# Kernel optimization log

Hardware: AMD Instinct MI355X
Metric: run time of the kernel (lower is better)

## Reference

```python
import jax, jax.numpy as jnp
import numpy as np

N_NODES = 50000
N_EDGES = 800000


def setup_inputs() -> dict:
    key = jax.random.key(0)
    ks = jax.random.split(key, 8)
    x = jax.random.normal(ks[0], (N_NODES, 256), dtype=jnp.float32)
    edge_index = jax.random.randint(ks[1], (2, N_EDGES), 0, N_NODES, dtype=jnp.int64)
    edge_weight = jax.random.uniform(ks[2], (N_EDGES,), dtype=jnp.float32)
    # Glorot-style weights for the 3 GCNConv layers: 256->128->64->32
    def glorot(k, fan_in, fan_out):
        s = jnp.sqrt(6.0 / (fan_in + fan_out))
        return jax.random.uniform(k, (fan_in, fan_out), dtype=jnp.float32, minval=-s, maxval=s)
    return {
        "x": x,
        "edge_index": edge_index,
        "edge_weight": edge_weight,
        "W1": glorot(ks[3], 256, 128), "b1": jnp.zeros((128,), jnp.float32),
        "W2": glorot(ks[4], 128, 64),  "b2": jnp.zeros((64,), jnp.float32),
        "W3": glorot(ks[5], 64, 32),   "b3": jnp.zeros((32,), jnp.float32),
    }


def _gcn_forward(x, row, col, ew, params):
    """Stacked GCNConv+ReLU (PyG semantics: add self loops, symmetric norm)."""
    n = x.shape[0]
    loop = jnp.arange(n, dtype=row.dtype)
    row_f = jnp.concatenate([row, loop])            # [E+N] sources
    col_f = jnp.concatenate([col, loop])            # [E+N] targets
    ew_f = jnp.concatenate([ew, jnp.ones((n,), ew.dtype)])
    deg = jax.ops.segment_sum(ew_f, col_f, num_segments=n)
    dinv = jnp.where(deg > 0, jax.lax.rsqrt(deg), 0.0)
    norm = dinv[row_f] * ew_f * dinv[col_f]         # [E+N]
    for W, b in params:
        h = x @ W                                   # [N, d_out] linear first (PyG order)
        msg = h[row_f] * norm[:, None]              # [E+N, d_out] gather + scale
        agg = jax.ops.segment_sum(msg, col_f, num_segments=n)  # scatter-add
        x = jax.nn.relu(agg + b)                    # fused bias + ReLU
    return x


def reference(x, edge_index, edge_weight, W1, b1, W2, b2, W3, b3):
    row, col = edge_index[0], edge_index[1]
    params = [(W1, b1), (W2, b2), (W3, b3)]
    return _gcn_forward(x, row, col, edge_weight, params)
```

## Files before the change

kernel.cpp:

```cpp
#include <hip/hip_runtime.h>
#include <hip/hip_fp16.h>


#define D0 256
#define D1 128
#define D2 64
#define D3 32

#define FIX_SCALE 16777216.0f
#define FIX_INV   (1.0f / 16777216.0f)

typedef _Float16 half8 __attribute__((ext_vector_type(8)));
typedef float floatx4 __attribute__((ext_vector_type(4)));

__global__ __launch_bounds__(256) void hist_kernel(
        const int* __restrict__ ei, const float* __restrict__ ew,
        unsigned long long* __restrict__ pk, int* __restrict__ rank, int E) {
    int e = blockIdx.x * 256 + threadIdx.x;
    if (e < E) {
        int c = ei[E + e];
        unsigned int wfix = (unsigned int)(ew[e] * FIX_SCALE + 0.5f);
        unsigned long long old =
            atomicAdd(&pk[c], (1ULL << 32) | (unsigned long long)wfix);
        rank[e] = (int)(old >> 32);
    }
}

__global__ __launch_bounds__(256) void scan_reduce(const unsigned long long* __restrict__ pk,
                                                   float* __restrict__ dinv,
                                                   int* __restrict__ cnt,
                                                   int* __restrict__ blockSum, int N) {
    __shared__ int s[256];
    const int t = threadIdx.x;
    const int i = blockIdx.x * 256 + t;
    int v = 0;
    if (i < N) {
        unsigned long long p = pk[i];
        float d = (float)(unsigned int)(p & 0xffffffffULL) * FIX_INV + 1.0f;
        dinv[i] = rsqrtf(d);
        v = (int)(p >> 32);
        cnt[i] = v;
    }
    s[t] = v;
    __syncthreads();
#pragma unroll
    for (int off = 128; off > 0; off >>= 1) {
        if (t < off) s[t] += s[t + off];
        __syncthreads();
    }
    if (t == 0) blockSum[blockIdx.x] = s[0];
}

__global__ __launch_bounds__(256) void scan_apply(const int* __restrict__ cnt,
                                                  const int* __restrict__ blockSum,
                                                  int* __restrict__ row_ptr, int N, int B) {
    __shared__ int bs[256];
    __shared__ int s[256];
    const int t = threadIdx.x;
    bs[t] = (t < B) ? blockSum[t] : 0;
    __syncthreads();
#pragma unroll
    for (int off = 1; off < 256; off <<= 1) {
        int u = (t >= off) ? bs[t - off] : 0;
        __syncthreads();
        bs[t] += u;
        __syncthreads();
    }
    const int myOff = (blockIdx.x > 0) ? bs[blockIdx.x - 1] : 0;
    const int i = blockIdx.x * 256 + t;
    const int v = (i < N) ? cnt[i] : 0;
    s[t] = v;
    __syncthreads();
#pragma unroll
    for (int off = 1; off < 256; off <<= 1) {
        int u = (t >= off) ? s[t - off] : 0;
        __syncthreads();
        s[t] += u;
        __syncthreads();
    }
    if (i < N) row_ptr[i] = s[t] - v + myOff;
    if (blockIdx.x == 0 && t == 0) row_ptr[N] = bs[B - 1];
}

__device__ __forceinline__ void stage_slab(const float* __restrict__ X, int slab,
                                           _Float16 (*__restrict__ sA)[D0 + 8], int t) {
    const int row = t >> 4;
    const int c0 = (t & 15) * 16;
    const float* src = X + (size_t)(slab * 16 + row) * D0 + c0;
    float4 f0 = *(const float4*)(src + 0);
    float4 f1 = *(const float4*)(src + 4);
    float4 f2 = *(const float4*)(src + 8);
    float4 f3 = *(const float4*)(src + 12);
    half8 h0, h1;
    h0[0] = (_Float16)f0.x; h0[1] = (_Float16)f0.y;
    h0[2] = (_Float16)f0.z; h0[3] = (_Float16)f0.w;
    h0[4] = (_Float16)f1.x; h0[5] = (_Float16)f1.y;
    h0[6] = (_Float16)f1.z; h0[7] = (_Float16)f1.w;
    h1[0] = (_Float16)f2.x; h1[1] = (_Float16)f2.y;
    h1[2] = (_Float16)f2.z; h1[3] = (_Float16)f2.w;
    h1[4] = (_Float16)f3.x; h1[5] = (_Float16)f3.y;
    h1[6] = (_Float16)f3.z; h1[7] = (_Float16)f3.w;
    *(half8*)&sA[row][c0]     = h0;
    *(half8*)&sA[row][c0 + 8] = h1;
}

__global__ __launch_bounds__(256) void fillgemm_kernel(
        const float* __restrict__ x, const float* __restrict__ W1,
        _Float16* __restrict__ h1, int N,
        const int* __restrict__ ei, const float* __restrict__ ew,
        const float* __restrict__ dinv, const int* __restrict__ row_ptr,
        const int* __restrict__ rank, int2* __restrict__ pairs, int E, int gB) {
    __shared__ _Float16 sA[2][16][D0 + 8];
    const int b = blockIdx.x;
    if (b >= gB) {
        int e = (b - gB) * 256 + threadIdx.x;
        if (e < E) {
            int r = ei[e];
            int c = ei[E + e];
            float w = dinv[r] * ew[e] * dinv[c];
            pairs[row_ptr[c] + rank[e]] = make_int2(r, __float_as_int(w));
        }
        return;
    }
    constexpr int NC = D0 / 32;
    const int tid = threadIdx.x;
    const int w = tid >> 6;
    const int lane = tid & 63;
    const int quad = lane >> 4;
    const int m = lane & 15;
    const int n0 = w * 32;

    half8 b0[NC], b1[NC];
#pragma unroll
    for (int c = 0; c < NC; ++c) {
#pragma unroll
        for (int j = 0; j < 8; ++j) {
            int k = c * 32 + quad * 8 + j;
            b0[c][j] = (_Float16)W1[(size_t)k * D1 + n0 + m];
            b1[c][j] = (_Float16)W1[(size_t)k * D1 + n0 + 16 + m];
        }
    }

    const int nslab = N >> 4;
    int slab = b;
    if (slab >= nslab) return;
    stage_slab(x, slab, sA[0], tid);
    __syncthreads();
    int buf = 0;
    while (true) {
        const int next = slab + gB;
        if (next < nslab) stage_slab(x, next, sA[buf ^ 1], tid);

        half8 a[NC];
#pragma unroll
        for (int c = 0; c < NC; ++c)
            a[c] = *(const half8*)&sA[buf][m][c * 32 + quad * 8];
        floatx4 acc0 = (floatx4){0.f, 0.f, 0.f, 0.f};
        floatx4 acc1 = (floatx4){0.f, 0.f, 0.f, 0.f};
#pragma unroll
        for (int c = 0; c < NC; ++c) {
            acc0 = __builtin_amdgcn_mfma_f32_16x16x32_f16(a[c], b0[c], acc0, 0, 0, 0);
            acc1 = __builtin_amdgcn_mfma_f32_16x16x32_f16(a[c], b1[c], acc1, 0, 0, 0);
        }

        const int r0 = slab * 16 + quad * 4;
#pragma unroll
        for (int r = 0; r < 4; ++r) {
            h1[(size_t)(r0 + r) * D1 + n0 + m]      = (_Float16)acc0[r];
            h1[(size_t)(r0 + r) * D1 + n0 + 16 + m] = (_Float16)acc1[r];
        }
        __syncthreads();
        if (next >= nslab) break;
        slab = next;
        buf ^= 1;
    }
}

template <int DIN, int DOUT>
__global__ __launch_bounds__(256) void agg_gemm_kernel(
        const _Float16* __restrict__ H, const int* __restrict__ row_ptr,
        const int2* __restrict__ pairs, const float* __restrict__ dinv,
        const float* __restrict__ bias, const float* __restrict__ W,
        _Float16* __restrict__ Hout, int N) {
    constexpr int TPN = DIN / 8;
    constexpr int NPB = 256 / TPN;
    constexpr int NC  = DIN / 32;
    constexpr int S   = NPB / 16;
    constexpr int T   = DOUT / 16;
    static_assert(S * T == 4, "one tile per wave");
    __shared__ _Float16 sA[NPB][DIN + 8];

    const int tid = threadIdx.x;
    const int g = tid / TPN;
    const int sl = tid % TPN;
    const int node0 = blockIdx.x * NPB;
    const int node = node0 + g;
    const bool valid = node < N;

    const int w = tid >> 6;
    const int lane = tid & 63;
    const int q = lane >> 4;
    const int m = lane & 15;
    const int s = w & (S - 1);
    const int t = w / S;
    half8 bf[NC];
#pragma unroll
    for (int c = 0; c < NC; ++c) {
#pragma unroll
        for (int j = 0; j < 8; ++j)
            bf[c][j] = (_Float16)W[(size_t)(c * 32 + q * 8 + j) * DOUT + t * 16 + m];
    }

    float acc[8];
#pragma unroll
    for (int j = 0; j < 8; ++j) acc[j] = 0.0f;

    int beg = 0, end = 0;
    float di = 0.f;
    half8 uself = (half8){0,0,0,0,0,0,0,0};
    float bb[8];
    if (valid) {
        beg = row_ptr[node];
        end = row_ptr[node + 1];
        di = dinv[node];
        uself = *(const half8*)&H[(size_t)node * DIN + sl * 8];
        *(float4*)&bb[0] = *(const float4*)&bias[sl * 8];
        *(float4*)&bb[4] = *(const float4*)&bias[sl * 8 + 4];
    }

    if (end > beg) {
        const int last = end - 1;
        int2 p0 = pairs[beg];
        int2 p1 = pairs[min(beg + 1, last)];
        int2 p2 = pairs[min(beg + 2, last)];
        int2 p3 = pairs[min(beg + 3, last)];
        int2 p4 = pairs[min(beg + 4, last)];
        half8 u0 = *(const half8*)&H[(size_t)p0.x * DIN + sl * 8];
        half8 u1 = *(const half8*)&H[(size_t)p1.x * DIN + sl * 8];
        half8 u2 = *(const half8*)&H[(size_t)p2.x * DIN + sl * 8];
        half8 u3 = *(const half8*)&H[(size_t)p3.x * DIN + sl * 8];
        for (int k = beg; k < end; ++k) {
            int2 p5 = pairs[min(k + 5, last)];
            half8 u4 = *(const half8*)&H[(size_t)p4.x * DIN + sl * 8];
            float wv = __int_as_float(p0.y);
#pragma unroll
            for (int j = 0; j < 8; ++j) acc[j] = fmaf(wv, (float)u0[j], acc[j]);
            p0 = p1; p1 = p2; p2 = p3; p3 = p4; p4 = p5;
            u0 = u1; u1 = u2; u2 = u3; u3 = u4;
        }
    }

    if (valid) {
        float d2 = di * di;
#pragma unroll
        for (int j = 0; j < 8; ++j) acc[j] = fmaf(d2, (float)uself[j], acc[j]);
        half8 o;
#pragma unroll
        for (int j = 0; j < 8; ++j) o[j] = (_Float16)fmaxf(acc[j] + bb[j], 0.f);
        *(half8*)&sA[g][sl * 8] = o;
    }
    __syncthreads();

    half8 a[NC];
#pragma unroll
    for (int c = 0; c < NC; ++c)
        a[c] = *(const half8*)&sA[s * 16 + m][c * 32 + q * 8];
    floatx4 o4 = (floatx4){0.f, 0.f, 0.f, 0.f};
#pragma unroll
    for (int c = 0; c < NC; ++c)
        o4 = __builtin_amdgcn_mfma_f32_16x16x32_f16(a[c], bf[c], o4, 0, 0, 0);
#pragma unroll
    for (int r = 0; r < 4; ++r) {
        const int nr = node0 + s * 16 + q * 4 + r;
        if (nr < N) Hout[(size_t)nr * DOUT + t * 16 + m] = (_Float16)o4[r];
    }
}

template <int D, typename OUT>
__global__ __launch_bounds__(256) void agg_kernel(const _Float16* __restrict__ H,
                                                  const int* __restrict__ row_ptr,
                                                  const int2* __restrict__ pairs,
                                                  const float* __restrict__ dinv,
                                                  const float* __restrict__ bias,
                                                  OUT* __restrict__ out, int N) {
    constexpr int TPN = D / 8;
    constexpr int NPB = 256 / TPN;
    const int tid = threadIdx.x;
    const int g = tid / TPN;
    const int lane = tid % TPN;
    const int node = blockIdx.x * NPB + g;
    if (node >= N) return;

    const int beg = row_ptr[node];
    const int end = row_ptr[node + 1];
    const float di = dinv[node];
    const half8 uself = *(const half8*)&H[(size_t)node * D + lane * 8];
    float b[8];
    *(float4*)&b[0] = *(const float4*)&bias[lane * 8];
    *(float4*)&b[4] = *(const float4*)&bias[lane * 8 + 4];

    float acc[8];
#pragma unroll
    for (int j = 0; j < 8; ++j) acc[j] = 0.0f;

    if (end > beg) {
        const int last = end - 1;
        int2 p0 = pairs[beg];
        int2 p1 = pairs[min(beg + 1, last)];
        int2 p2 = pairs[min(beg + 2, last)];
        int2 p3 = pairs[min(beg + 3, last)];
        int2 p4 = pairs[min(beg + 4, last)];
        half8 u0 = *(const half8*)&H[(size_t)p0.x * D + lane * 8];
        half8 u1 = *(const half8*)&H[(size_t)p1.x * D + lane * 8];
        half8 u2 = *(const half8*)&H[(size_t)p2.x * D + lane * 8];
        half8 u3 = *(const half8*)&H[(size_t)p3.x * D + lane * 8];
        for (int k = beg; k < end; ++k) {
            int2 p5 = pairs[min(k + 5, last)];
            half8 u4 = *(const half8*)&H[(size_t)p4.x * D + lane * 8];
            float w = __int_as_float(p0.y);
#pragma unroll
            for (int j = 0; j < 8; ++j) acc[j] = fmaf(w, (float)u0[j], acc[j]);
            p0 = p1; p1 = p2; p2 = p3; p3 = p4; p4 = p5;
            u0 = u1; u1 = u2; u2 = u3; u3 = u4;
        }
    }
    const float d2 = di * di;
#pragma unroll
    for (int j = 0; j < 8; ++j) acc[j] = fmaf(d2, (float)uself[j], acc[j]);
#pragma unroll
    for (int j = 0; j < 8; ++j) acc[j] = fmaxf(acc[j] + b[j], 0.f);

    if constexpr (sizeof(OUT) == 2) {
        half8 o;
#pragma unroll
        for (int j = 0; j < 8; ++j) o[j] = (_Float16)acc[j];
        *(half8*)&out[(size_t)node * D + lane * 8] = o;
    } else {
        float* dst = (float*)&out[(size_t)node * D + lane * 8];
        *(float4*)&dst[0] = make_float4(acc[0], acc[1], acc[2], acc[3]);
        *(float4*)&dst[4] = make_float4(acc[4], acc[5], acc[6], acc[7]);
    }
}

extern "C" void kernel_launch(void* const* d_in, const int* in_sizes, int n_in,
                              void* d_out, int out_size, void* d_ws, size_t ws_size,
                              hipStream_t stream) {
    const float* x   = (const float*)d_in[0];
    const int* ei    = (const int*)d_in[1];
    const float* ew  = (const float*)d_in[2];
    const float* W1  = (const float*)d_in[3];
    const float* b1  = (const float*)d_in[4];
    const float* W2  = (const float*)d_in[5];
    const float* b2  = (const float*)d_in[6];
    const float* W3  = (const float*)d_in[7];
    const float* b3  = (const float*)d_in[8];
    float* out = (float*)d_out;

    const int N = in_sizes[0] / D0;
    const int E = in_sizes[2];
    (void)n_in; (void)out_size; (void)ws_size;

    char* ws = (char*)d_ws;
    size_t off = 0;
    auto carve = [&](size_t bytes) -> void* {
        void* p = (void*)(ws + off);
        off += (bytes + 255) & ~(size_t)255;
        return p;
    };
    unsigned long long* pk = (unsigned long long*)carve((size_t)N * 8);
    float* dinv    = (float*)carve((size_t)N * 4);
    int*   cnt     = (int*)carve((size_t)N * 4);
    int*   row_ptr = (int*)carve((size_t)(N + 1) * 4);
    int*   rank    = (int*)carve((size_t)E * 4);
    int*   bsum    = (int*)carve(256 * 4);
    int2*  pairs   = (int2*)carve((size_t)E * 8);
    _Float16* bufH = (_Float16*)carve((size_t)N * D1 * 2);
    _Float16* bufO = (_Float16*)carve((size_t)N * D1 * 2);

    _Float16* h1 = bufH;
    _Float16* h2 = bufO;
    _Float16* h3 = bufH;

    const int eb = (E + 255) / 256;
    const int scanB = (N + 255) / 256;
    const int gB = 768;

    hipMemsetAsync(pk, 0, (size_t)N * 8, stream);
    hist_kernel<<<eb, 256, 0, stream>>>(ei, ew, pk, rank, E);

    scan_reduce<<<scanB, 256, 0, stream>>>(pk, dinv, cnt, bsum, N);
    scan_apply<<<scanB, 256, 0, stream>>>(cnt, bsum, row_ptr, N, scanB);

    fillgemm_kernel<<<gB + eb, 256, 0, stream>>>(
        x, W1, h1, N, ei, ew, dinv, row_ptr, rank, pairs, E, gB);

    agg_gemm_kernel<D1, D2><<<(N + 15) / 16, 256, 0, stream>>>(
        h1, row_ptr, pairs, dinv, b1, W2, h2, N);

    agg_gemm_kernel<D2, D3><<<(N + 31) / 32, 256, 0, stream>>>(
        h2, row_ptr, pairs, dinv, b2, W3, h3, N);

    agg_kernel<D3, float><<<(N + 63) / 64, 256, 0, stream>>>(
        h3, row_ptr, pairs, dinv, b3, out, N);
}
```

Baseline: 253.9 us.

## Sort nodes by degree for aggregation and overlap histogram with first GEMM

Builds a degree-bucketed permutation of nodes (counting sort over in-degree) so that aggregation kernels process nodes of similar degree together, reducing warp divergence and load imbalance from uneven neighbour counts. It also moves the edge histogram into the first GEMM kernel launch, running it alongside the first GEMM, and splits the edge fill into its own kernel. This adds extra launches (perm scan, scatter, fill), an indirection through perm on every node read and output write, and scattered output stores.

```diff
diff --git a/kernel.cpp b/kernel.cpp
--- a/kernel.cpp
+++ b/kernel.cpp
@@ -9,78 +9,10 @@
 
 #define FIX_SCALE 16777216.0f
 #define FIX_INV   (1.0f / 16777216.0f)
+#define SCANB_MAX 200
 
 typedef _Float16 half8 __attribute__((ext_vector_type(8)));
 typedef float floatx4 __attribute__((ext_vector_type(4)));
-
-__global__ __launch_bounds__(256) void hist_kernel(
-        const int* __restrict__ ei, const float* __restrict__ ew,
-        unsigned long long* __restrict__ pk, int* __restrict__ rank, int E) {
-    int e = blockIdx.x * 256 + threadIdx.x;
-    if (e < E) {
-        int c = ei[E + e];
-        unsigned int wfix = (unsigned int)(ew[e] * FIX_SCALE + 0.5f);
-        unsigned long long old =
-            atomicAdd(&pk[c], (1ULL << 32) | (unsigned long long)wfix);
-        rank[e] = (int)(old >> 32);
-    }
-}
-
-__global__ __launch_bounds__(256) void scan_reduce(const unsigned long long* __restrict__ pk,
-                                                   float* __restrict__ dinv,
-                                                   int* __restrict__ cnt,
-                                                   int* __restrict__ blockSum, int N) {
-    __shared__ int s[256];
-    const int t = threadIdx.x;
-    const int i = blockIdx.x * 256 + t;
-    int v = 0;
-    if (i < N) {
-        unsigned long long p = pk[i];
-        float d = (float)(unsigned int)(p & 0xffffffffULL) * FIX_INV + 1.0f;
-        dinv[i] = rsqrtf(d);
-        v = (int)(p >> 32);
-        cnt[i] = v;
-    }
-    s[t] = v;
-    __syncthreads();
-#pragma unroll
-    for (int off = 128; off > 0; off >>= 1) {
-        if (t < off) s[t] += s[t + off];
-        __syncthreads();
-    }
-    if (t == 0) blockSum[blockIdx.x] = s[0];
-}
-
-__global__ __launch_bounds__(256) void scan_apply(const int* __restrict__ cnt,
-                                                  const int* __restrict__ blockSum,
-                                                  int* __restrict__ row_ptr, int N, int B) {
-    __shared__ int bs[256];
-    __shared__ int s[256];
-    const int t = threadIdx.x;
-    bs[t] = (t < B) ? blockSum[t] : 0;
-    __syncthreads();
-#pragma unroll
-    for (int off = 1; off < 256; off <<= 1) {
-        int u = (t >= off) ? bs[t - off] : 0;
-        __syncthreads();
-        bs[t] += u;
-        __syncthreads();
-    }
-    const int myOff = (blockIdx.x > 0) ? bs[blockIdx.x - 1] : 0;
-    const int i = blockIdx.x * 256 + t;
-    const int v = (i < N) ? cnt[i] : 0;
-    s[t] = v;
-    __syncthreads();
-#pragma unroll
-    for (int off = 1; off < 256; off <<= 1) {
-        int u = (t >= off) ? s[t - off] : 0;
-        __syncthreads();
-        s[t] += u;
-        __syncthreads();
-    }
-    if (i < N) row_ptr[i] = s[t] - v + myOff;
-    if (blockIdx.x == 0 && t == 0) row_ptr[N] = bs[B - 1];
-}
 
 __device__ __forceinline__ void stage_slab(const float* __restrict__ X, int slab,
                                            _Float16 (*__restrict__ sA)[D0 + 8], int t) {
@@ -104,21 +36,22 @@
     *(half8*)&sA[row][c0 + 8] = h1;
 }
 
-__global__ __launch_bounds__(256) void fillgemm_kernel(
+__global__ __launch_bounds__(256) void hist_gemm1_kernel(
         const float* __restrict__ x, const float* __restrict__ W1,
         _Float16* __restrict__ h1, int N,
         const int* __restrict__ ei, const float* __restrict__ ew,
-        const float* __restrict__ dinv, const int* __restrict__ row_ptr,
-        const int* __restrict__ rank, int2* __restrict__ pairs, int E, int gB) {
+        unsigned long long* __restrict__ pk, int* __restrict__ rank, int E,
+        int gB) {
     __shared__ _Float16 sA[2][16][D0 + 8];
     const int b = blockIdx.x;
     if (b >= gB) {
         int e = (b - gB) * 256 + threadIdx.x;
         if (e < E) {
-            int r = ei[e];
             int c = ei[E + e];
-            float w = dinv[r] * ew[e] * dinv[c];
-            pairs[row_ptr[c] + rank[e]] = make_int2(r, __float_as_int(w));
+            unsigned int wfix = (unsigned int)(ew[e] * FIX_SCALE + 0.5f);
+            unsigned long long old =
+                atomicAdd(&pk[c], (1ULL << 32) | (unsigned long long)wfix);
+            rank[e] = (int)(old >> 32);
         }
         return;
     }
@@ -176,11 +109,139 @@
     }
 }
 
+__global__ __launch_bounds__(256) void scan_reduce(const unsigned long long* __restrict__ pk,
+                                                   float* __restrict__ dinv,
+                                                   int* __restrict__ cnt,
+                                                   int* __restrict__ blockSum,
+                                                   int* __restrict__ blockHist, int N) {
+    __shared__ int s[256];
+    __shared__ int bh[64];
+    const int t = threadIdx.x;
+    const int i = blockIdx.x * 256 + t;
+    if (t < 64) bh[t] = 0;
+    int v = 0;
+    if (i < N) {
+        unsigned long long p = pk[i];
+        float d = (float)(unsigned int)(p & 0xffffffffULL) * FIX_INV + 1.0f;
+        dinv[i] = rsqrtf(d);
+        v = (int)(p >> 32);
+        cnt[i] = v;
+    }
+    __syncthreads();
+    if (i < N) atomicAdd(&bh[min(v, 63)], 1);
+    s[t] = v;
+    __syncthreads();
+#pragma unroll
+    for (int off = 128; off > 0; off >>= 1) {
+        if (t < off) s[t] += s[t + off];
+        __syncthreads();
+    }
+    if (t == 0) blockSum[blockIdx.x] = s[0];
+    if (t < 64) blockHist[blockIdx.x * 64 + t] = bh[t];
+}
+
+__global__ __launch_bounds__(256) void scan_apply(const int* __restrict__ cnt,
+                                                  const int* __restrict__ blockSum,
+                                                  int* __restrict__ row_ptr, int N, int B) {
+    __shared__ int bs[256];
+    __shared__ int s[256];
+    const int t = threadIdx.x;
+    bs[t] = (t < B) ? blockSum[t] : 0;
+    __syncthreads();
+#pragma unroll
+    for (int off = 1; off < 256; off <<= 1) {
+        int u = (t >= off) ? bs[t - off] : 0;
+        __syncthreads();
+        bs[t] += u;
+        __syncthreads();
+    }
+    const int myOff = (blockIdx.x > 0) ? bs[blockIdx.x - 1] : 0;
+    const int i = blockIdx.x * 256 + t;
+    const int v = (i < N) ? cnt[i] : 0;
+    s[t] = v;
+    __syncthreads();
+#pragma unroll
+    for (int off = 1; off < 256; off <<= 1) {
+        int u = (t >= off) ? s[t - off] : 0;
+        __syncthreads();
+        s[t] += u;
+        __syncthreads();
+    }
+    if (i < N) row_ptr[i] = s[t] - v + myOff;
+    if (blockIdx.x == 0 && t == 0) row_ptr[N] = bs[B - 1];
+}
+
+__global__ __launch_bounds__(256) void perm_scan(const int* __restrict__ bh,
+                                                 int* __restrict__ gbase,
+                                                 int B) {
+    __shared__ int v[64 * SCANB_MAX];
+    __shared__ int ps[256];
+    const int t = threadIdx.x;
+    const int tot = 64 * B;
+    for (int i = t; i < tot; i += 256) {
+        int d = i / B, b = i - d * B;
+        v[i] = bh[b * 64 + d];
+    }
+    __syncthreads();
+    const int chunk = (tot + 255) / 256;
+    const int lo = t * chunk;
+    const int hi = min(lo + chunk, tot);
+    int sum = 0;
+    for (int i = lo; i < hi; ++i) sum += v[i];
+    ps[t] = sum;
+    __syncthreads();
+#pragma unroll
+    for (int off = 1; off < 256; off <<= 1) {
+        int u = (t >= off) ? ps[t - off] : 0;
+        __syncthreads();
+        ps[t] += u;
+        __syncthreads();
+    }
+    int run = (t > 0) ? ps[t - 1] : 0;
+    for (int i = lo; i < hi; ++i) { int x = v[i]; v[i] = run; run += x; }
+    __syncthreads();
+    for (int i = t; i < tot; i += 256) gbase[i] = v[i];
+}
+
+__global__ __launch_bounds__(256) void perm_scatter(const int* __restrict__ cnt,
+                                                    const int* __restrict__ gbase,
+                                                    int* __restrict__ perm, int N, int B) {
+    __shared__ int c[64];
+    const int t = threadIdx.x;
+    if (t < 64) c[t] = 0;
+    __syncthreads();
+    const int i = blockIdx.x * 256 + t;
+    if (i < N) {
+        int d = min(cnt[i], 63);
+        int pos = atomicAdd(&c[d], 1);
+        perm[gbase[d * B + blockIdx.x] + pos] = i;
+    }
+}
+
+__global__ void perm_ident(int* __restrict__ perm, int N) {
+    int i = blockIdx.x * blockDim.x + threadIdx.x;
+    if (i < N) perm[i] = i;
+}
+
+__global__ void fill_kernel(const int* __restrict__ ei, const float* __restrict__ ew,
+                            const float* __restrict__ dinv,
+                            const int* __restrict__ row_ptr, const int* __restrict__ rank,
+                            int2* __restrict__ pairs, int E) {
+    int e = blockIdx.x * blockDim.x + threadIdx.x;
+    if (e < E) {
+        int r = ei[e];
+        int c = ei[E + e];
+        float w = dinv[r] * ew[e] * dinv[c];
+        pairs[row_ptr[c] + rank[e]] = make_int2(r, __float_as_int(w));
+    }
+}
+
 template <int DIN, int DOUT>
 __global__ __launch_bounds__(256) void agg_gemm_kernel(
         const _Float16* __restrict__ H, const int* __restrict__ row_ptr,
         const int2* __restrict__ pairs, const float* __restrict__ dinv,
         const float* __restrict__ bias, const float* __restrict__ W,
+        const int* __restrict__ perm,
         _Float16* __restrict__ Hout, int N) {
     constexpr int TPN = DIN / 8;
     constexpr int NPB = 256 / TPN;
@@ -194,8 +255,8 @@
     const int g = tid / TPN;
     const int sl = tid % TPN;
     const int node0 = blockIdx.x * NPB;
-    const int node = node0 + g;
-    const bool valid = node < N;
+    const bool valid = (node0 + g) < N;
+    const int node = valid ? perm[node0 + g] : 0;
 
     const int w = tid >> 6;
     const int lane = tid & 63;
@@ -271,8 +332,9 @@
         o4 = __builtin_amdgcn_mfma_f32_16x16x32_f16(a[c], bf[c], o4, 0, 0, 0);
 #pragma unroll
     for (int r = 0; r < 4; ++r) {
-        const int nr = node0 + s * 16 + q * 4 + r;
-        if (nr < N) Hout[(size_t)nr * DOUT + t * 16 + m] = (_Float16)o4[r];
+        const int slot = node0 + s * 16 + q * 4 + r;
+        if (slot < N)
+            Hout[(size_t)perm[slot] * DOUT + t * 16 + m] = (_Float16)o4[r];
     }
 }
 
@@ -282,14 +344,16 @@
                                                   const int2* __restrict__ pairs,
                                                   const float* __restrict__ dinv,
                                                   const float* __restrict__ bias,
+                                                  const int* __restrict__ perm,
                                                   OUT* __restrict__ out, int N) {
     constexpr int TPN = D / 8;
     constexpr int NPB = 256 / TPN;
     const int tid = threadIdx.x;
     const int g = tid / TPN;
     const int lane = tid % TPN;
-    const int node = blockIdx.x * NPB + g;
-    if (node >= N) return;
+    const int slot = blockIdx.x * NPB + g;
+    if (slot >= N) return;
+    const int node = perm[slot];
 
     const int beg = row_ptr[node];
     const int end = row_ptr[node + 1];
@@ -373,6 +437,9 @@
     int*   row_ptr = (int*)carve((size_t)(N + 1) * 4);
     int*   rank    = (int*)carve((size_t)E * 4);
     int*   bsum    = (int*)carve(256 * 4);
+    int*   bhist   = (int*)carve((size_t)SCANB_MAX * 64 * 4);
+    int*   gbase   = (int*)carve((size_t)SCANB_MAX * 64 * 4);
+    int*   perm    = (int*)carve((size_t)N * 4);
     int2*  pairs   = (int2*)carve((size_t)E * 8);
     _Float16* bufH = (_Float16*)carve((size_t)N * D1 * 2);
     _Float16* bufO = (_Float16*)carve((size_t)N * D1 * 2);
@@ -386,20 +453,27 @@
     const int gB = 768;
 
     hipMemsetAsync(pk, 0, (size_t)N * 8, stream);
-    hist_kernel<<<eb, 256, 0, stream>>>(ei, ew, pk, rank, E);
-
-    scan_reduce<<<scanB, 256, 0, stream>>>(pk, dinv, cnt, bsum, N);
+    hist_gemm1_kernel<<<gB + eb, 256, 0, stream>>>(
+        x, W1, h1, N, ei, ew, pk, rank, E, gB);
+
+    scan_reduce<<<scanB, 256, 0, stream>>>(pk, dinv, cnt, bsum, bhist, N);
     scan_apply<<<scanB, 256, 0, stream>>>(cnt, bsum, row_ptr, N, scanB);
 
-    fillgemm_kernel<<<gB + eb, 256, 0, stream>>>(
-        x, W1, h1, N, ei, ew, dinv, row_ptr, rank, pairs, E, gB);
+    if (scanB <= SCANB_MAX) {
+        perm_scan<<<1, 256, 0, stream>>>(bhist, gbase, scanB);
+        perm_scatter<<<scanB, 256, 0, stream>>>(cnt, gbase, perm, N, scanB);
+    } else {
+        perm_ident<<<scanB, 256, 0, stream>>>(perm, N);
+    }
+
+    fill_kernel<<<eb, 256, 0, stream>>>(ei, ew, dinv, row_ptr, rank, pairs, E);
 
     agg_gemm_kernel<D1, D2><<<(N + 15) / 16, 256, 0, stream>>>(
-        h1, row_ptr, pairs, dinv, b1, W2, h2, N);
+        h1, row_ptr, pairs, dinv, b1, W2, perm, h2, N);
 
     agg_gemm_kernel<D2, D3><<<(N + 31) / 32, 256, 0, stream>>>(
-        h2, row_ptr, pairs, dinv, b2, W3, h3, N);
+        h2, row_ptr, pairs, dinv, b2, W3, perm, h3, N);
 
     agg_kernel<D3, float><<<(N + 63) / 64, 256, 0, stream>>>(
-        h3, row_ptr, pairs, dinv, b3, out, N);
-}
+        h3, row_ptr, pairs, dinv, b3, perm, out, N);
+}
```

Measured after the change: 267.9 us. 5.5% more time.
